# Kernel optimization log

Measured on AMD Instinct MI355X. Metric: run time of the kernel, lower is better.

## Reference

```python
import jax, jax.numpy as jnp
import numpy as np

EMB_DIM = 400
NUM_ENT = 100000
NUM_REL = 200
OUT_CH = 6
STRIDE = 2
MAX_ARITY = 3
ARITY = 3
BATCH = 8192
W_OUT = (EMB_DIM - 1) // STRIDE + 1          # conv output width (filt_w=1, stride=2)
FC_LEN = OUT_CH * W_OUT                      # 1200


def setup_inputs() -> dict:
    key = jax.random.key(0)
    ks = jax.random.split(key, 10)
    r_idx = jax.random.randint(ks[0], (BATCH,), 0, NUM_REL)
    E_mat = jax.random.randint(ks[1], (BATCH, ARITY), 0, NUM_ENT)
    ms = jax.random.normal(ks[2], (BATCH, ARITY), dtype=jnp.float32)
    bs = jax.random.normal(ks[3], (BATCH, ARITY), dtype=jnp.float32)
    E_emb = jax.random.normal(ks[4], (NUM_ENT, EMB_DIM), dtype=jnp.float32) * 0.05
    R_emb = jax.random.normal(ks[5], (NUM_REL, EMB_DIM), dtype=jnp.float32) * 0.05
    fc2_W = jax.random.normal(ks[6], (OUT_CH, MAX_ARITY + 1), dtype=jnp.float32) * 0.1
    fc2_b = jax.random.normal(ks[7], (OUT_CH,), dtype=jnp.float32) * 0.1
    fc_W = jax.random.normal(ks[8], (EMB_DIM, FC_LEN), dtype=jnp.float32) * 0.02
    fc_b = jax.random.normal(ks[9], (EMB_DIM,), dtype=jnp.float32) * 0.02
    return {"r_idx": r_idx, "E_mat": E_mat, "ms": ms, "bs": bs,
            "E_emb": E_emb, "R_emb": R_emb,
            "fc2_W": fc2_W, "fc2_b": fc2_b, "fc_W": fc_W, "fc_b": fc_b}


def _convolve(E_emb, fc2_W, fc2_b, fc_W, fc_b, e_idx, pos):
    # Embedding gather: (B, D)
    e = E_emb[e_idx]
    # 1x1 grouped conv with stride=2 == strided slice of the embedding: (B, W_OUT)
    e_s = e[:, ::STRIDE]
    # Hypernetwork filter from fc2(one_hot(pos)) -- identical across batch: (OUT_CH,)
    k = fc2_W[:, pos] + fc2_b
    # Per-sample outer product, flattened oc-major (matches torch view order): (B, FC_LEN)
    feat = (k[None, :, None] * e_s[:, None, :]).reshape(e.shape[0], FC_LEN)
    # fc: Linear(FC_LEN, EMB_DIM)
    return jnp.einsum('bf,df->bd', feat, fc_W) + fc_b


def reference(r_idx, E_mat, ms, bs, E_emb, R_emb, fc2_W, fc2_b, fc_W, fc_b):
    r = R_emb[r_idx]                                        # (B, D)
    x = None
    for i in range(E_mat.shape[1]):                         # small fixed arity loop
        e = _convolve(E_emb, fc2_W, fc2_b, fc_W, fc_b, E_mat[:, i], i)
        e = e * ms[:, i][:, None] + bs[:, i][:, None]
        x = e if x is None else x * e
    x = x * r
    return jnp.sum(x, axis=1)                               # (B,)
```

## Files before the change

### kernel.cpp

```cpp
#include <hip/hip_runtime.h>

typedef __attribute__((ext_vector_type(8))) short bf16x8;
typedef __attribute__((ext_vector_type(4))) float f32x4;

#define EMB_DIM 400
#define OUT_CH  6
#define ARITY   3
#define BATCH   8192
#define W_OUT   200
#define FC_LEN  1200
#define NT      25
#define NKS     7
#define BM      32

static __device__ __forceinline__ ushort f2bf(float f) {
    union { float f; uint u; } v; v.f = f;
    uint u = v.u;
    return (ushort)((u + 0x7FFF + ((u >> 16) & 1)) >> 16);
}

__global__ __launch_bounds__(256)
void pack_M(const float* __restrict__ fc2_W, const float* __restrict__ fc2_b,
            const float* __restrict__ fc_W, ushort* __restrict__ Mb) {
    __shared__ float Bt[224][16];
    const int bid = blockIdx.x;
    const int i = bid / NT, t = bid % NT;
    float kc[OUT_CH];
#pragma unroll
    for (int c = 0; c < OUT_CH; ++c) kc[c] = fc2_W[c * 4 + i] + fc2_b[c];
    const int tid = threadIdx.x;
    const int dd = tid >> 4, wl = tid & 15;
    const int d = t * 16 + dd;
#pragma unroll
    for (int s = 0; s < 14; ++s) {
        int w = wl + 16 * s;
        float v = 0.f;
        if (w < W_OUT) {
#pragma unroll
            for (int c = 0; c < OUT_CH; ++c)
                v = fmaf(kc[c], fc_W[d * FC_LEN + c * W_OUT + w], v);
        }
        Bt[w][dd] = v;
    }
    __syncthreads();
    const int l = tid & 63;
    for (int kk = tid >> 6; kk < NKS; kk += 4) {
        ushort vals[8];
#pragma unroll
        for (int j = 0; j < 8; ++j)
            vals[j] = f2bf(Bt[kk * 32 + (l >> 4) * 8 + j][l & 15]);
        *reinterpret_cast<uint4*>(Mb + ((size_t)(bid * NKS + kk) * 64 + l) * 8) =
            *reinterpret_cast<const uint4*>(vals);
    }
}

__global__ __launch_bounds__(512)
void hype_mfma(const int* __restrict__ r_idx, const int* __restrict__ E_mat,
               const float* __restrict__ ms, const float* __restrict__ bs,
               const float* __restrict__ E_emb, const float* __restrict__ R_emb,
               const float* __restrict__ fc_b, const ushort* __restrict__ Mb,
               float* __restrict__ out) {
    __shared__ ushort es[ARITY * 2 * NKS * 64 * 8];
    __shared__ float sm_ms[BM * 3], sm_bs[BM * 3], sm_fcb[EMB_DIM];
    __shared__ int   sm_rb[BM];
    __shared__ float osum[4][BM];

    const int tid = threadIdx.x;
    const int b0 = blockIdx.x * BM;

    if (tid < BM * 3) { sm_ms[tid] = ms[b0 * 3 + tid]; sm_bs[tid] = bs[b0 * 3 + tid]; }
    if (tid >= 96 && tid < 96 + BM) sm_rb[tid - 96] = r_idx[b0 + tid - 96] * EMB_DIM;
    if (tid >= 112 && tid < 112 + EMB_DIM) sm_fcb[tid - 112] = fc_b[tid - 112];

    uint* esu = reinterpret_cast<uint*>(es);
    for (int z = tid; z < ARITY * 2 * 192; z += 512) {
        int pair = z / 192, off = z % 192;
        esu[(pair * NKS + 6) * 256 + 64 + off] = 0;
    }
    for (int tq = tid; tq < ARITY * BM * 100; tq += 512) {
        int q = tq % 100;
        int p = tq / 100;
        int i = p / BM, r = p % BM;
        int ent = E_mat[(b0 + r) * ARITY + i];
        const float4 v = *reinterpret_cast<const float4*>(E_emb + (size_t)ent * EMB_DIM + 4 * q);
        int w = 2 * q;
        int kk = w >> 5;
        int lsub = (w >> 3) & 3;
        int j = w & 7;
        int rg = r >> 4, rl = r & 15;
        int l = lsub * 16 + rl;
        uint pk = (uint)f2bf(v.x) | ((uint)f2bf(v.z) << 16);
        esu[(((i * 2 + rg) * NKS + kk) * 64 + l) * 4 + (j >> 1)] = pk;
    }
    __syncthreads();

    const int wid = tid >> 6;
    const int lane = tid & 63;
    const int rg = wid & 1, cg = wid >> 1;
    const int cl = lane & 15;
    const int rql = lane >> 4;

    bf16x8 afrag[ARITY][NKS];
#pragma unroll
    for (int i = 0; i < ARITY; ++i)
#pragma unroll
        for (int kk = 0; kk < NKS; ++kk)
            afrag[i][kk] = *reinterpret_cast<const bf16x8*>(
                es + (((i * 2 + rg) * NKS + kk) * 64 + lane) * 8);

    float msv[ARITY][4], bsv[ARITY][4];
    int rbv[4];
#pragma unroll
    for (int r_ = 0; r_ < 4; ++r_) {
        int row = rg * 16 + rql * 4 + r_;
#pragma unroll
        for (int i = 0; i < ARITY; ++i) {
            msv[i][r_] = sm_ms[row * 3 + i];
            bsv[i][r_] = sm_bs[row * 3 + i];
        }
        rbv[r_] = sm_rb[row];
    }

    float rowsum[4] = {0.f, 0.f, 0.f, 0.f};
    for (int t = cg; t < NT; t += 4) {
        f32x4 acc[ARITY];
#pragma unroll
        for (int i = 0; i < ARITY; ++i) {
            f32x4 a = {0.f, 0.f, 0.f, 0.f};
            const ushort* bp = Mb + ((size_t)(i * NT + t) * NKS * 64 + lane) * 8;
#pragma unroll
            for (int kk = 0; kk < NKS; ++kk) {
                bf16x8 bfr = *reinterpret_cast<const bf16x8*>(bp + kk * 512);
                a = __builtin_amdgcn_mfma_f32_16x16x32_bf16(afrag[i][kk], bfr, a, 0, 0, 0);
            }
            acc[i] = a;
        }
        const int d = t * 16 + cl;
        const float fcb = sm_fcb[d];
#pragma unroll
        for (int r_ = 0; r_ < 4; ++r_) {
            float Rr = R_emb[rbv[r_] + d];
            float e0 = fmaf(acc[0][r_] + fcb, msv[0][r_], bsv[0][r_]);
            float e1 = fmaf(acc[1][r_] + fcb, msv[1][r_], bsv[1][r_]);
            float e2 = fmaf(acc[2][r_] + fcb, msv[2][r_], bsv[2][r_]);
            rowsum[r_] = fmaf(e0 * e1 * e2, Rr, rowsum[r_]);
        }
    }

#pragma unroll
    for (int m = 1; m < 16; m <<= 1)
#pragma unroll
        for (int r_ = 0; r_ < 4; ++r_)
            rowsum[r_] += __shfl_xor(rowsum[r_], m, 64);
    if (cl == 0) {
#pragma unroll
        for (int r_ = 0; r_ < 4; ++r_)
            osum[cg][rg * 16 + rql * 4 + r_] = rowsum[r_];
    }
    __syncthreads();
    if (tid < BM)
        out[b0 + tid] = osum[0][tid] + osum[1][tid] + osum[2][tid] + osum[3][tid];
}

extern "C" void kernel_launch(void* const* d_in, const int* in_sizes, int n_in,
                              void* d_out, int out_size, void* d_ws, size_t ws_size,
                              hipStream_t stream) {
    const int*   r_idx = (const int*)d_in[0];
    const int*   E_mat = (const int*)d_in[1];
    const float* ms    = (const float*)d_in[2];
    const float* bs    = (const float*)d_in[3];
    const float* E_emb = (const float*)d_in[4];
    const float* R_emb = (const float*)d_in[5];
    const float* fc2_W = (const float*)d_in[6];
    const float* fc2_b = (const float*)d_in[7];
    const float* fc_W  = (const float*)d_in[8];
    const float* fc_b  = (const float*)d_in[9];
    float*  out = (float*)d_out;
    ushort* Mb  = (ushort*)d_ws;

    pack_M<<<ARITY * NT, 256, 0, stream>>>(fc2_W, fc2_b, fc_W, Mb);
    hype_mfma<<<BATCH / BM, 512, 0, stream>>>(r_idx, E_mat, ms, bs, E_emb, R_emb,
                                              fc_b, Mb, out);
}
```

Measured before the change: 36.13 us.

## Split column tiles across two grid halves with smaller row blocks and atomic output

```diff
diff --git a/kernel.cpp b/kernel.cpp
--- a/kernel.cpp
+++ b/kernel.cpp
@@ -11,7 +11,7 @@
 #define FC_LEN  1200
 #define NT      25
 #define NKS     7
-#define BM      32
+#define BM      16
 
 static __device__ __forceinline__ ushort f2bf(float f) {
     union { float f; uint u; } v; v.f = f;
@@ -22,8 +22,9 @@
 __global__ __launch_bounds__(256)
 void pack_M(const float* __restrict__ fc2_W, const float* __restrict__ fc2_b,
             const float* __restrict__ fc_W, ushort* __restrict__ Mb) {
-    __shared__ float Bt[224][16];
+    __shared__ float Bt[112][16];
     const int bid = blockIdx.x;
+    const int h   = blockIdx.y;
     const int i = bid / NT, t = bid % NT;
     float kc[OUT_CH];
 #pragma unroll
@@ -32,52 +33,55 @@
     const int dd = tid >> 4, wl = tid & 15;
     const int d = t * 16 + dd;
 #pragma unroll
-    for (int s = 0; s < 14; ++s) {
-        int w = wl + 16 * s;
+    for (int s = 0; s < 7; ++s) {
+        int w = 112 * h + wl + 16 * s;
         float v = 0.f;
         if (w < W_OUT) {
 #pragma unroll
             for (int c = 0; c < OUT_CH; ++c)
                 v = fmaf(kc[c], fc_W[d * FC_LEN + c * W_OUT + w], v);
         }
-        Bt[w][dd] = v;
+        Bt[w - 112 * h][dd] = v;
     }
     __syncthreads();
     const int l = tid & 63;
     for (int kk = tid >> 6; kk < NKS; kk += 4) {
+        int w0 = kk * 32 + (l >> 4) * 8;
+        if (w0 < 112 * h || w0 >= 112 * h + 112) continue;
         ushort vals[8];
 #pragma unroll
         for (int j = 0; j < 8; ++j)
-            vals[j] = f2bf(Bt[kk * 32 + (l >> 4) * 8 + j][l & 15]);
+            vals[j] = f2bf(Bt[w0 - 112 * h + j][l & 15]);
         *reinterpret_cast<uint4*>(Mb + ((size_t)(bid * NKS + kk) * 64 + l) * 8) =
             *reinterpret_cast<const uint4*>(vals);
     }
 }
 
-__global__ __launch_bounds__(512)
+__global__ __launch_bounds__(256, 4)
 void hype_mfma(const int* __restrict__ r_idx, const int* __restrict__ E_mat,
                const float* __restrict__ ms, const float* __restrict__ bs,
                const float* __restrict__ E_emb, const float* __restrict__ R_emb,
                const float* __restrict__ fc_b, const ushort* __restrict__ Mb,
                float* __restrict__ out) {
-    __shared__ ushort es[ARITY * 2 * NKS * 64 * 8];
+    __shared__ ushort es[ARITY * NKS * 64 * 8];
     __shared__ float sm_ms[BM * 3], sm_bs[BM * 3], sm_fcb[EMB_DIM];
     __shared__ int   sm_rb[BM];
     __shared__ float osum[4][BM];
 
     const int tid = threadIdx.x;
     const int b0 = blockIdx.x * BM;
+    const int split = blockIdx.y;
 
     if (tid < BM * 3) { sm_ms[tid] = ms[b0 * 3 + tid]; sm_bs[tid] = bs[b0 * 3 + tid]; }
-    if (tid >= 96 && tid < 96 + BM) sm_rb[tid - 96] = r_idx[b0 + tid - 96] * EMB_DIM;
-    if (tid >= 112 && tid < 112 + EMB_DIM) sm_fcb[tid - 112] = fc_b[tid - 112];
+    if (tid >= 64 && tid < 64 + BM) sm_rb[tid - 64] = r_idx[b0 + tid - 64] * EMB_DIM;
+    for (int z = tid; z < EMB_DIM; z += 256) sm_fcb[z] = fc_b[z];
 
     uint* esu = reinterpret_cast<uint*>(es);
-    for (int z = tid; z < ARITY * 2 * 192; z += 512) {
-        int pair = z / 192, off = z % 192;
-        esu[(pair * NKS + 6) * 256 + 64 + off] = 0;
+    for (int z = tid; z < ARITY * 192; z += 256) {
+        int i = z / 192, off = z % 192;
+        esu[(i * NKS + 6) * 256 + 64 + off] = 0;
     }
-    for (int tq = tid; tq < ARITY * BM * 100; tq += 512) {
+    for (int tq = tid; tq < ARITY * BM * 100; tq += 256) {
         int q = tq % 100;
         int p = tq / 100;
         int i = p / BM, r = p % BM;
@@ -87,16 +91,14 @@
         int kk = w >> 5;
         int lsub = (w >> 3) & 3;
         int j = w & 7;
-        int rg = r >> 4, rl = r & 15;
-        int l = lsub * 16 + rl;
+        int l = lsub * 16 + r;
         uint pk = (uint)f2bf(v.x) | ((uint)f2bf(v.z) << 16);
-        esu[(((i * 2 + rg) * NKS + kk) * 64 + l) * 4 + (j >> 1)] = pk;
+        esu[((i * NKS + kk) * 64 + l) * 4 + (j >> 1)] = pk;
     }
     __syncthreads();
 
-    const int wid = tid >> 6;
+    const int cg = tid >> 6;
     const int lane = tid & 63;
-    const int rg = wid & 1, cg = wid >> 1;
     const int cl = lane & 15;
     const int rql = lane >> 4;
 
@@ -106,23 +108,11 @@
 #pragma unroll
         for (int kk = 0; kk < NKS; ++kk)
             afrag[i][kk] = *reinterpret_cast<const bf16x8*>(
-                es + (((i * 2 + rg) * NKS + kk) * 64 + lane) * 8);
+                es + ((i * NKS + kk) * 64 + lane) * 8);
 
-    float msv[ARITY][4], bsv[ARITY][4];
-    int rbv[4];
-#pragma unroll
-    for (int r_ = 0; r_ < 4; ++r_) {
-        int row = rg * 16 + rql * 4 + r_;
-#pragma unroll
-        for (int i = 0; i < ARITY; ++i) {
-            msv[i][r_] = sm_ms[row * 3 + i];
-            bsv[i][r_] = sm_bs[row * 3 + i];
-        }
-        rbv[r_] = sm_rb[row];
-    }
-
+    const int cgp = split + 2 * cg;
     float rowsum[4] = {0.f, 0.f, 0.f, 0.f};
-    for (int t = cg; t < NT; t += 4) {
+    for (int t = cgp; t < NT; t += 8) {
         f32x4 acc[ARITY];
 #pragma unroll
         for (int i = 0; i < ARITY; ++i) {
@@ -139,10 +129,11 @@
         const float fcb = sm_fcb[d];
 #pragma unroll
         for (int r_ = 0; r_ < 4; ++r_) {
-            float Rr = R_emb[rbv[r_] + d];
-            float e0 = fmaf(acc[0][r_] + fcb, msv[0][r_], bsv[0][r_]);
-            float e1 = fmaf(acc[1][r_] + fcb, msv[1][r_], bsv[1][r_]);
-            float e2 = fmaf(acc[2][r_] + fcb, msv[2][r_], bsv[2][r_]);
+            int row = rql * 4 + r_;
+            float Rr = R_emb[sm_rb[row] + d];
+            float e0 = fmaf(acc[0][r_] + fcb, sm_ms[row * 3 + 0], sm_bs[row * 3 + 0]);
+            float e1 = fmaf(acc[1][r_] + fcb, sm_ms[row * 3 + 1], sm_bs[row * 3 + 1]);
+            float e2 = fmaf(acc[2][r_] + fcb, sm_ms[row * 3 + 2], sm_bs[row * 3 + 2]);
             rowsum[r_] = fmaf(e0 * e1 * e2, Rr, rowsum[r_]);
         }
     }
@@ -155,11 +146,13 @@
     if (cl == 0) {
 #pragma unroll
         for (int r_ = 0; r_ < 4; ++r_)
-            osum[cg][rg * 16 + rql * 4 + r_] = rowsum[r_];
+            osum[cg][rql * 4 + r_] = rowsum[r_];
     }
     __syncthreads();
-    if (tid < BM)
-        out[b0 + tid] = osum[0][tid] + osum[1][tid] + osum[2][tid] + osum[3][tid];
+    if (tid < BM) {
+        float s = osum[0][tid] + osum[1][tid] + osum[2][tid] + osum[3][tid];
+        atomicAdd(&out[b0 + tid], s);
+    }
 }
 
 extern "C" void kernel_launch(void* const* d_in, const int* in_sizes, int n_in,
@@ -178,7 +171,8 @@
     float*  out = (float*)d_out;
     ushort* Mb  = (ushort*)d_ws;
 
-    pack_M<<<ARITY * NT, 256, 0, stream>>>(fc2_W, fc2_b, fc_W, Mb);
-    hype_mfma<<<BATCH / BM, 512, 0, stream>>>(r_idx, E_mat, ms, bs, E_emb, R_emb,
-                                              fc_b, Mb, out);
+    hipMemsetAsync(out, 0, (size_t)out_size * sizeof(float), stream);
+    pack_M<<<dim3(ARITY * NT, 2), 256, 0, stream>>>(fc2_W, fc2_b, fc_W, Mb);
+    hype_mfma<<<dim3(BATCH / BM, 2), 256, 0, stream>>>(r_idx, E_mat, ms, bs, E_emb,
+                                                       R_emb, fc_b, Mb, out);
 }
```

Result: slower. 53.74 us (+48.7%).

## Batch embedding gathers into registers and split pack_M across K-slices

Applied to the files above, without the earlier changes.

```diff
diff --git a/kernel.cpp b/kernel.cpp
--- a/kernel.cpp
+++ b/kernel.cpp
@@ -12,6 +12,8 @@
 #define NT      25
 #define NKS     7
 #define BM      32
+#define NTASK   (ARITY * BM * 100)
+#define NLD     19
 
 static __device__ __forceinline__ ushort f2bf(float f) {
     union { float f; uint u; } v; v.f = f;
@@ -22,8 +24,9 @@
 __global__ __launch_bounds__(256)
 void pack_M(const float* __restrict__ fc2_W, const float* __restrict__ fc2_b,
             const float* __restrict__ fc_W, ushort* __restrict__ Mb) {
-    __shared__ float Bt[224][16];
+    __shared__ float Bt[32][16];
     const int bid = blockIdx.x;
+    const int kk  = blockIdx.y;
     const int i = bid / NT, t = bid % NT;
     float kc[OUT_CH];
 #pragma unroll
@@ -32,23 +35,23 @@
     const int dd = tid >> 4, wl = tid & 15;
     const int d = t * 16 + dd;
 #pragma unroll
-    for (int s = 0; s < 14; ++s) {
-        int w = wl + 16 * s;
+    for (int s = 0; s < 2; ++s) {
+        int w = kk * 32 + wl + 16 * s;
         float v = 0.f;
         if (w < W_OUT) {
 #pragma unroll
             for (int c = 0; c < OUT_CH; ++c)
                 v = fmaf(kc[c], fc_W[d * FC_LEN + c * W_OUT + w], v);
         }
-        Bt[w][dd] = v;
-    }
-    __syncthreads();
-    const int l = tid & 63;
-    for (int kk = tid >> 6; kk < NKS; kk += 4) {
+        Bt[wl + 16 * s][dd] = v;
+    }
+    __syncthreads();
+    if (tid < 64) {
+        const int l = tid;
         ushort vals[8];
 #pragma unroll
         for (int j = 0; j < 8; ++j)
-            vals[j] = f2bf(Bt[kk * 32 + (l >> 4) * 8 + j][l & 15]);
+            vals[j] = f2bf(Bt[(l >> 4) * 8 + j][l & 15]);
         *reinterpret_cast<uint4*>(Mb + ((size_t)(bid * NKS + kk) * 64 + l) * 8) =
             *reinterpret_cast<const uint4*>(vals);
     }
@@ -62,35 +65,56 @@
                float* __restrict__ out) {
     __shared__ ushort es[ARITY * 2 * NKS * 64 * 8];
     __shared__ float sm_ms[BM * 3], sm_bs[BM * 3], sm_fcb[EMB_DIM];
-    __shared__ int   sm_rb[BM];
+    __shared__ int   sm_rb[BM], sm_ent[BM * 3];
     __shared__ float osum[4][BM];
 
     const int tid = threadIdx.x;
     const int b0 = blockIdx.x * BM;
 
-    if (tid < BM * 3) { sm_ms[tid] = ms[b0 * 3 + tid]; sm_bs[tid] = bs[b0 * 3 + tid]; }
+    if (tid < BM * 3) {
+        sm_ms[tid]  = ms[b0 * 3 + tid];
+        sm_bs[tid]  = bs[b0 * 3 + tid];
+        sm_ent[tid] = E_mat[b0 * 3 + tid];
+    }
     if (tid >= 96 && tid < 96 + BM) sm_rb[tid - 96] = r_idx[b0 + tid - 96] * EMB_DIM;
-    if (tid >= 112 && tid < 112 + EMB_DIM) sm_fcb[tid - 112] = fc_b[tid - 112];
+    for (int z = tid; z < EMB_DIM; z += 512) sm_fcb[z] = fc_b[z];
 
     uint* esu = reinterpret_cast<uint*>(es);
     for (int z = tid; z < ARITY * 2 * 192; z += 512) {
         int pair = z / 192, off = z % 192;
         esu[(pair * NKS + 6) * 256 + 64 + off] = 0;
     }
-    for (int tq = tid; tq < ARITY * BM * 100; tq += 512) {
-        int q = tq % 100;
-        int p = tq / 100;
-        int i = p / BM, r = p % BM;
-        int ent = E_mat[(b0 + r) * ARITY + i];
-        const float4 v = *reinterpret_cast<const float4*>(E_emb + (size_t)ent * EMB_DIM + 4 * q);
-        int w = 2 * q;
-        int kk = w >> 5;
-        int lsub = (w >> 3) & 3;
-        int j = w & 7;
-        int rg = r >> 4, rl = r & 15;
-        int l = lsub * 16 + rl;
-        uint pk = (uint)f2bf(v.x) | ((uint)f2bf(v.z) << 16);
-        esu[(((i * 2 + rg) * NKS + kk) * 64 + l) * 4 + (j >> 1)] = pk;
+    __syncthreads();
+
+    float4 vreg[NLD];
+#pragma unroll
+    for (int k = 0; k < NLD; ++k) {
+        int tq = tid + k * 512;
+        if (tq < NTASK) {
+            int q = tq % 100;
+            int p = tq / 100;
+            int i = p / BM, r = p % BM;
+            int ent = sm_ent[r * 3 + i];
+            vreg[k] = *reinterpret_cast<const float4*>(
+                E_emb + (size_t)ent * EMB_DIM + 4 * q);
+        }
+    }
+#pragma unroll
+    for (int k = 0; k < NLD; ++k) {
+        int tq = tid + k * 512;
+        if (tq < NTASK) {
+            int q = tq % 100;
+            int p = tq / 100;
+            int i = p / BM, r = p % BM;
+            int w = 2 * q;
+            int kk = w >> 5;
+            int lsub = (w >> 3) & 3;
+            int j = w & 7;
+            int rg = r >> 4, rl = r & 15;
+            int l = lsub * 16 + rl;
+            uint pk = (uint)f2bf(vreg[k].x) | ((uint)f2bf(vreg[k].z) << 16);
+            esu[(((i * 2 + rg) * NKS + kk) * 64 + l) * 4 + (j >> 1)] = pk;
+        }
     }
     __syncthreads();
 
@@ -178,7 +202,7 @@
     float*  out = (float*)d_out;
     ushort* Mb  = (ushort*)d_ws;
 
-    pack_M<<<ARITY * NT, 256, 0, stream>>>(fc2_W, fc2_b, fc_W, Mb);
+    pack_M<<<dim3(ARITY * NT, NKS), 256, 0, stream>>>(fc2_W, fc2_b, fc_W, Mb);
     hype_mfma<<<BATCH / BM, 512, 0, stream>>>(r_idx, E_mat, ms, bs, E_emb, R_emb,
                                               fc_b, Mb, out);
 }
```

Result: faster. 34.08 us (-5.7%).
